# Performance work log

Hardware: AMD Instinct MI355X
Metric: run time of the kernel (lower is better)

Reference implementation:

```python
import jax, jax.numpy as jnp
import numpy as np

N_A = N_B = N_C = 50000
E = 800000
D_IN = 256
D_OUT = 128
T_ATT = 64


def _spmm(row, col, val, ft, n_dst):
    # sparse [n_dst, n_src] @ ft : gather src rows, scale, scatter-add to dst
    return jax.ops.segment_sum(val[:, None] * ft[col], row, num_segments=n_dst)


def setup_inputs() -> dict:
    key = jax.random.key(0)
    ks = jax.random.split(key, 40)
    f32 = jnp.float32
    inp = {
        'x_a': jax.random.normal(ks[0], (N_A, D_IN), f32),
        'x_b': jax.random.normal(ks[1], (N_B, D_IN), f32),
        'x_c': jax.random.normal(ks[2], (N_C, D_IN), f32),
    }
    # COO adjacency per relation: (dst_row, src_col, value)
    rel = {'ab': (N_A, N_B), 'ac': (N_A, N_C), 'ba': (N_B, N_A), 'ca': (N_C, N_A)}
    i = 3
    for name, (nd, ns) in rel.items():
        inp['row_' + name] = jax.random.randint(ks[i], (E,), 0, nd); i += 1
        inp['col_' + name] = jax.random.randint(ks[i], (E,), 0, ns); i += 1
        inp['val_' + name] = jax.random.uniform(ks[i], (E,), f32); i += 1
    # learned parameters (xavier-ish scale)
    def w(k, shape, s=0.05):
        return jax.random.normal(k, shape, f32) * s
    inp['w_self_a'] = w(ks[i], (D_IN, D_OUT)); i += 1
    inp['w_self_b'] = w(ks[i], (D_IN, D_OUT)); i += 1
    inp['w_self_c'] = w(ks[i], (D_IN, D_OUT)); i += 1
    inp['W_ab'] = w(ks[i], (D_IN, D_OUT)); i += 1
    inp['W_ac'] = w(ks[i], (D_IN, D_OUT)); i += 1
    inp['W_ba'] = w(ks[i], (D_IN, D_OUT)); i += 1
    inp['W_ca'] = w(ks[i], (D_IN, D_OUT)); i += 1
    inp['bias_a'] = w(ks[i], (1, D_OUT)); i += 1
    inp['bias_b'] = w(ks[i], (1, D_OUT)); i += 1
    inp['bias_c'] = w(ks[i], (1, D_OUT)); i += 1
    inp['w_cat_a'] = w(ks[i], (2 * D_OUT, D_OUT)); i += 1
    inp['w_cat_b'] = w(ks[i], (2 * D_OUT, D_OUT)); i += 1
    inp['w_cat_c'] = w(ks[i], (2 * D_OUT, D_OUT)); i += 1
    inp['w_query_a'] = w(ks[i], (D_OUT, T_ATT)); i += 1
    inp['w_keys_a'] = w(ks[i], (D_OUT, T_ATT)); i += 1
    inp['w_att_a'] = w(ks[i], (2 * T_ATT, 1)); i += 1
    return inp


def reference(x_a, x_b, x_c,
              row_ab, col_ab, val_ab, row_ac, col_ac, val_ac,
              row_ba, col_ba, val_ba, row_ca, col_ca, val_ca,
              w_self_a, w_self_b, w_self_c,
              W_ab, W_ac, W_ba, W_ca,
              bias_a, bias_b, bias_c,
              w_cat_a, w_cat_b, w_cat_c,
              w_query_a, w_keys_a, w_att_a):
    # ---- type 'a': neighbors [b, c], attention fusion ----
    self_a = x_a @ w_self_a                                   # [Na, D]
    nb_b = _spmm(row_ab, col_ab, val_ab, x_b @ W_ab, N_A)     # [Na, D]
    nb_c = _spmm(row_ac, col_ac, val_ac, x_c @ W_ac, N_A)     # [Na, D]
    q = self_a @ w_query_a                                    # [Na, T]
    e_b = jax.nn.elu(jnp.concatenate([nb_b @ w_keys_a, q], 1) @ w_att_a)  # [Na, 1]
    e_c = jax.nn.elu(jnp.concatenate([nb_c @ w_keys_a, q], 1) @ w_att_a)  # [Na, 1]
    att = jax.nn.softmax(jnp.concatenate([e_b, e_c], 1), axis=1)          # [Na, 2]
    agg_a = nb_b * att[:, :1] + nb_c * att[:, 1:2]
    out_a = jnp.concatenate([agg_a, self_a], 1) @ w_cat_a + bias_a
    # ---- type 'b': single neighbor 'a' ----
    self_b = x_b @ w_self_b
    agg_b = _spmm(row_ba, col_ba, val_ba, x_a @ W_ba, N_B)
    out_b = jnp.concatenate([agg_b, self_b], 1) @ w_cat_b + bias_b
    # ---- type 'c': single neighbor 'a' ----
    self_c = x_c @ w_self_c
    agg_c = _spmm(row_ca, col_ca, val_ca, x_a @ W_ca, N_C)
    out_c = jnp.concatenate([agg_c, self_c], 1) @ w_cat_c + bias_c
    # concat per-type outputs (all D_OUT wide) into one array
    return jnp.concatenate([out_a, out_b, out_c], 0)          # [Na+Nb+Nc, D]
```

## Files before the change

kernel.cpp:

```cpp
#include <hip/hip_runtime.h>

#define NA 50000
#define NE 800000
#define NBKT 196
#define CAP 4608
#define BSTRIDE (NBKT * CAP)

typedef unsigned int   u32;
typedef unsigned short u16;
typedef short s16x8 __attribute__((ext_vector_type(8)));
typedef float f32x4 __attribute__((ext_vector_type(4)));

__device__ __forceinline__ u16 f2bf(float f) {
  u32 u = __float_as_uint(f);
  u += 0x7fffu + ((u >> 16) & 1u);
  return (u16)(u >> 16);
}

__device__ __forceinline__ void acc8(float* a, uint4 q, float v) {
  a[0] += v * __uint_as_float(q.x << 16);
  a[1] += v * __uint_as_float(q.x & 0xffff0000u);
  a[2] += v * __uint_as_float(q.y << 16);
  a[3] += v * __uint_as_float(q.y & 0xffff0000u);
  a[4] += v * __uint_as_float(q.z << 16);
  a[5] += v * __uint_as_float(q.z & 0xffff0000u);
  a[6] += v * __uint_as_float(q.w << 16);
  a[7] += v * __uint_as_float(q.w & 0xffff0000u);
}

__device__ __forceinline__ void glds16(const u16* g, u16* l) {
  __builtin_amdgcn_global_load_lds(
      (const __attribute__((address_space(1))) u32*)g,
      (__attribute__((address_space(3))) u32*)l, 16, 0, 0);
}

struct Rel4 { const int* row[4]; const int* col[4]; const float* val[4]; };

struct Prep {
  const float* src[10]; u16* dst[10];
  const float* wq; const float* wk; const float* wa; float* uvp;
  u32* gcur;
};

struct ConvArgs { const float* x[3]; u16* xb; };

struct FtArgs { const u16* A[3]; const u16* Bt[3]; u16* C[3]; };

struct FuseW { const u16* Wf[3]; const float* bias[3]; float* out[3]; };

__global__ __launch_bounds__(256) void k_prep(Prep P) {
  int gy = blockIdx.y;
  if (gy < 7) {
    int idx = blockIdx.x * 256 + threadIdx.x;
    int k = idx & 255, n = idx >> 8;
    P.dst[gy][n * 256 + k] = f2bf(P.src[gy][k * 128 + n]);
  } else if (gy < 10) {
    int idx = blockIdx.x * 256 + threadIdx.x;
    int e = idx & 7, l = (idx >> 3) & 63, jj = (idx >> 9) & 7, ks = idx >> 12;
    int n = jj * 16 + (l & 15);
    int k = ks * 32 + ((l >> 4) * 8) + e;
    P.dst[gy][idx] = f2bf(P.src[gy][k * 128 + n]);
  } else if (blockIdx.x == 0) {
    int t = threadIdx.x;
    int d = t & 127, which = t >> 7;
    const float* w = which ? P.wq : P.wk;
    const float* a = P.wa + which * 64;
    float s = 0.f;
    for (int i = 0; i < 64; ++i) s += w[d * 64 + i] * a[i];
    P.uvp[which * 128 + d] = s;
  } else if (blockIdx.x == 1) {
    for (int i = threadIdx.x; i < 1024; i += 256)
      P.gcur[i] = (u32)((i & 255) * CAP);
  }
}

__global__ __launch_bounds__(256) void k_main1(Rel4 R, u32* __restrict__ gcur,
                                               uint2* __restrict__ pairs, ConvArgs CA) {
  __shared__ __align__(16) char smem[40960];
  const int gy = blockIdx.y;
  const int t = threadIdx.x;
  if (gy < 4) {
    if (blockIdx.x >= 196) return;
    int rel = gy;
    int e0 = blockIdx.x * 4096;
    int nrem = min(4096, NE - e0);
    u32* sw0  = (u32*)smem;
    u32* sval = sw0 + 4096;
    unsigned char* sbkt = (unsigned char*)(sval + 4096);
    u32* hist  = (u32*)(sbkt + 4096);
    u32* lscan = hist + 256;
    u32* cnt2  = lscan + 256;
    u32* gbase = cnt2 + 256;
    hist[t] = 0; cnt2[t] = 0;
    __syncthreads();
    const int* rr = R.row[rel];
    const int* cc = R.col[rel];
    const float* vl = R.val[rel];
    u32 w0[16]; u32 vv[16]; int bb[16];
    #pragma unroll
    for (int i = 0; i < 16; ++i) {
      int li = t + i * 256;
      bool ok = li < nrem;
      int idx = e0 + (ok ? li : 0);
      int r = ok ? rr[idx] : 0;
      int c = ok ? cc[idx] : 0;
      float v = ok ? vl[idx] : 0.f;
      u32 b = (u32)r >> 8;
      w0[i] = (u32)(c & 0xFFFF) | ((u32)(r & 255) << 16) | (b << 24);
      vv[i] = __float_as_uint(v);
      bb[i] = ok ? (int)b : -1;
      if (ok) atomicAdd(&hist[b], 1u);
    }
    __syncthreads();
    lscan[t] = hist[t];
    __syncthreads();
    for (int ofs = 1; ofs < 256; ofs <<= 1) {
      u32 y = (t >= ofs) ? lscan[t - ofs] : 0u;
      __syncthreads();
      lscan[t] += y;
      __syncthreads();
    }
    gbase[t] = atomicAdd(&gcur[rel * 256 + t], hist[t]);
    #pragma unroll
    for (int i = 0; i < 16; ++i) {
      if (bb[i] >= 0) {
        int b = bb[i];
        u32 p = (lscan[b] - hist[b]) + atomicAdd(&cnt2[b], 1u);
        sw0[p] = w0[i]; sval[p] = vv[i]; sbkt[p] = (unsigned char)b;
      }
    }
    __syncthreads();
    uint2* P = pairs + (size_t)rel * BSTRIDE;
    #pragma unroll
    for (int i = 0; i < 16; ++i) {
      int p = t + i * 256;
      if (p < nrem) {
        int b = sbkt[p];
        u32 gd = gbase[b] + (u32)p - (lscan[b] - hist[b]);
        uint2 pr; pr.x = sw0[p]; pr.y = sval[p];
        P[gd] = pr;
      }
    }
  } else {
    const size_t TOT = 38400000;
    const size_t TSZ = 12800000;
    size_t base = ((size_t)(gy - 4) * 391 + blockIdx.x) * 16384 + (size_t)t * 8;
    #pragma unroll
    for (int it = 0; it < 8; ++it) {
      size_t g = base + (size_t)it * 2048;
      if (g < TOT) {
        int which = (g >= 2 * TSZ) ? 2 : (g >= TSZ ? 1 : 0);
        size_t off = g - (size_t)which * TSZ;
        const float* sp = CA.x[which] + off;
        float4 v0 = *(const float4*)(sp);
        float4 v1 = *(const float4*)(sp + 4);
        s16x8 o;
        o[0] = (short)f2bf(v0.x); o[1] = (short)f2bf(v0.y);
        o[2] = (short)f2bf(v0.z); o[3] = (short)f2bf(v0.w);
        o[4] = (short)f2bf(v1.x); o[5] = (short)f2bf(v1.y);
        o[6] = (short)f2bf(v1.z); o[7] = (short)f2bf(v1.w);
        *(s16x8*)(CA.xb + g) = o;
      }
    }
  }
}

__global__ __launch_bounds__(256) void k_main2(const u32* __restrict__ gcur,
    int* __restrict__ ofs_s, int* __restrict__ ofs_e,
    const uint2* __restrict__ pairs, u32* __restrict__ epak, FtArgs Ar) {
  __shared__ __align__(16) char smem[40960];
  const int gy = blockIdx.y;
  const int t = threadIdx.x;
  if (gy < 4) {
    if (blockIdx.x >= 196) return;
    int rel = gy;
    int b = blockIdx.x;
    int base = b * CAP;
    int n = (int)gcur[rel * 256 + b] - base;
    u32* sw0  = (u32*)smem;
    u32* sv   = sw0 + CAP;
    u32* hist = sv + CAP;
    u32* scan = hist + 256;
    u32* cur  = scan + 256;
    hist[t] = 0;
    __syncthreads();
    const uint2* P = pairs + (size_t)rel * BSTRIDE;
    for (int p = t; p < n; p += 256) {
      uint2 pr = P[base + p];
      sw0[p] = pr.x; sv[p] = pr.y;
      atomicAdd(&hist[(pr.x >> 16) & 255], 1u);
    }
    __syncthreads();
    u32 own = hist[t];
    scan[t] = own;
    __syncthreads();
    for (int ofs = 1; ofs < 256; ofs <<= 1) {
      u32 y = (t >= ofs) ? scan[t - ofs] : 0u;
      __syncthreads();
      scan[t] += y;
      __syncthreads();
    }
    u32 excl = scan[t] - own;
    cur[t] = excl;
    int r0 = b << 8;
    if (r0 + t < NA) {
      ofs_s[(size_t)rel * NA + r0 + t] = base + (int)excl;
      ofs_e[(size_t)rel * NA + r0 + t] = base + (int)(excl + own);
    }
    __syncthreads();
    u32* E = epak + (size_t)rel * BSTRIDE;
    for (int p = t; p < n; p += 256) {
      u32 w = sw0[p];
      int rl = (w >> 16) & 255;
      u32 d = atomicAdd(&cur[rl], 1u);
      E[base + (int)d] = (w & 0xFFFFu) | ((u32)f2bf(__uint_as_float(sv[p])) << 16);
    }
  } else {
    u16* Asl = (u16*)smem;
    u16* Bsl = Asl + 128 * 64;
    const int by = gy - 4;
    const int which = (by < 3) ? 0 : (by < 5 ? 1 : 2);
    const int col0 = (by - (which == 0 ? 0 : (which == 1 ? 3 : 5))) * 128;
    const int ldc = (which == 0) ? 384 : 256;
    const u16* A = Ar.A[which];
    const u16* Bt = Ar.Bt[which] + (size_t)col0 * 256;
    u16* C = Ar.C[which] + col0;
    const int row0 = blockIdx.x * 128;
    const int w = t >> 6, l = t & 63;
    const int wr = (w >> 1) * 64, wc = (w & 1) * 64;
    f32x4 acc[4][4] = {};
    for (int kk = 0; kk < 4; ++kk) {
      #pragma unroll
      for (int q = 0; q < 4; ++q) {
        int c = q * 256 + t;
        int r = c >> 3, col8 = (c & 7) * 8;
        int gr = row0 + r; gr = gr < NA ? gr : NA - 1;
        glds16(A + (size_t)gr * 256 + kk * 64 + col8, Asl + c * 8);
        glds16(Bt + (size_t)r * 256 + kk * 64 + col8, Bsl + c * 8);
      }
      __syncthreads();
      #pragma unroll
      for (int ks = 0; ks < 2; ++ks) {
        s16x8 af[4], bfr[4];
        #pragma unroll
        for (int i = 0; i < 4; ++i)
          af[i] = *(const s16x8*)&Asl[(wr + i * 16 + (l & 15)) * 64 + ks * 32 + (l >> 4) * 8];
        #pragma unroll
        for (int j = 0; j < 4; ++j)
          bfr[j] = *(const s16x8*)&Bsl[(wc + j * 16 + (l & 15)) * 64 + ks * 32 + (l >> 4) * 8];
        #pragma unroll
        for (int i = 0; i < 4; ++i)
          #pragma unroll
          for (int j = 0; j < 4; ++j)
            acc[i][j] = __builtin_amdgcn_mfma_f32_16x16x32_bf16(af[i], bfr[j], acc[i][j], 0, 0, 0);
      }
      __syncthreads();
    }
    #pragma unroll
    for (int i = 0; i < 4; ++i)
      #pragma unroll
      for (int j = 0; j < 4; ++j)
        #pragma unroll
        for (int q = 0; q < 4; ++q) {
          int r = row0 + wr + i * 16 + (l >> 4) * 4 + q;
          if (r < NA) C[(size_t)r * ldc + wc + j * 16 + (l & 15)] = f2bf(acc[i][j][q]);
        }
  }
}

__global__ __launch_bounds__(256) void k_spmm(
    const int* __restrict__ ofs_s, const int* __restrict__ ofs_e,
    const u32* __restrict__ epak,
    const u16* __restrict__ ya, const u16* __restrict__ yb, const u16* __restrict__ yc,
    const float* __restrict__ uv, FuseW FW) {
  __shared__ u16 Asm[16 * 264];
  int tid = threadIdx.x;
  int lane = tid & 63, wid = tid >> 6;
  int g = lane >> 4, gl = lane & 15;
  const u32 glb = (u32)gl * 16;
  int lr = wid * 4 + g;
  int row = blockIdx.x * 16 + lr;
  int gy = blockIdx.y;
  if (gy == 0) {
    const char* ybase = (const char*)yb;
    const char* cbase = (const char*)yc;
    float fb[8] = {0,0,0,0,0,0,0,0};
    float fc[8] = {0,0,0,0,0,0,0,0};
    {
      int i = ofs_s[row], e = ofs_e[row];
      for (; i + 4 <= e; i += 4) {
        u32 p0 = epak[i], p1 = epak[i + 1], p2 = epak[i + 2], p3 = epak[i + 3];
        uint4 q0 = *(const uint4*)(ybase + (((p0 & 0xFFFFu) << 9) + glb));
        uint4 q1 = *(const uint4*)(ybase + (((p1 & 0xFFFFu) << 9) + glb));
        uint4 q2 = *(const uint4*)(ybase + (((p2 & 0xFFFFu) << 9) + glb));
        uint4 q3 = *(const uint4*)(ybase + (((p3 & 0xFFFFu) << 9) + glb));
        acc8(fb, q0, __uint_as_float(p0 & 0xffff0000u));
        acc8(fb, q1, __uint_as_float(p1 & 0xffff0000u));
        acc8(fb, q2, __uint_as_float(p2 & 0xffff0000u));
        acc8(fb, q3, __uint_as_float(p3 & 0xffff0000u));
      }
      for (; i < e; ++i) {
        u32 p0 = epak[i];
        uint4 q0 = *(const uint4*)(ybase + (((p0 & 0xFFFFu) << 9) + glb));
        acc8(fb, q0, __uint_as_float(p0 & 0xffff0000u));
      }
    }
    {
      const u32* pr = epak + BSTRIDE;
      int i = ofs_s[NA + row], e = ofs_e[NA + row];
      for (; i + 4 <= e; i += 4) {
        u32 p0 = pr[i], p1 = pr[i + 1], p2 = pr[i + 2], p3 = pr[i + 3];
        uint4 q0 = *(const uint4*)(cbase + (((p0 & 0xFFFFu) << 9) + glb));
        uint4 q1 = *(const uint4*)(cbase + (((p1 & 0xFFFFu) << 9) + glb));
        uint4 q2 = *(const uint4*)(cbase + (((p2 & 0xFFFFu) << 9) + glb));
        uint4 q3 = *(const uint4*)(cbase + (((p3 & 0xFFFFu) << 9) + glb));
        acc8(fc, q0, __uint_as_float(p0 & 0xffff0000u));
        acc8(fc, q1, __uint_as_float(p1 & 0xffff0000u));
        acc8(fc, q2, __uint_as_float(p2 & 0xffff0000u));
        acc8(fc, q3, __uint_as_float(p3 & 0xffff0000u));
      }
      for (; i < e; ++i) {
        u32 p0 = pr[i];
        uint4 q0 = *(const uint4*)(cbase + (((p0 & 0xFFFFu) << 9) + glb));
        acc8(fc, q0, __uint_as_float(p0 & 0xffff0000u));
      }
    }
    uint4 sq = *(const uint4*)((const char*)ya + (u32)row * 768 + glb);
    float sf[8];
    sf[0] = __uint_as_float(sq.x << 16); sf[1] = __uint_as_float(sq.x & 0xffff0000u);
    sf[2] = __uint_as_float(sq.y << 16); sf[3] = __uint_as_float(sq.y & 0xffff0000u);
    sf[4] = __uint_as_float(sq.z << 16); sf[5] = __uint_as_float(sq.z & 0xffff0000u);
    sf[6] = __uint_as_float(sq.w << 16); sf[7] = __uint_as_float(sq.w & 0xffff0000u);
    float pb = 0.f, pc = 0.f, pq = 0.f;
    const float* up = uv + gl * 8;
    const float* vp = uv + 128 + gl * 8;
    #pragma unroll
    for (int j = 0; j < 8; ++j) {
      pb += fb[j] * up[j];
      pc += fc[j] * up[j];
      pq += sf[j] * vp[j];
    }
    #pragma unroll
    for (int off = 1; off < 16; off <<= 1) {
      pb += __shfl_xor(pb, off);
      pc += __shfl_xor(pc, off);
      pq += __shfl_xor(pq, off);
    }
    float eb = pb + pq, ec = pc + pq;
    eb = eb > 0.f ? eb : (expf(eb) - 1.f);
    ec = ec > 0.f ? ec : (expf(ec) - 1.f);
    float m = fmaxf(eb, ec);
    float p0 = expf(eb - m), p1 = expf(ec - m);
    float inv = 1.f / (p0 + p1);
    float a0 = p0 * inv, a1 = p1 * inv;
    s16x8 av;
    #pragma unroll
    for (int j = 0; j < 8; ++j) av[j] = (short)f2bf(a0 * fb[j] + a1 * fc[j]);
    *(s16x8*)&Asm[lr * 264 + gl * 8] = av;
    *(s16x8*)&Asm[lr * 264 + 128 + gl * 8] = *(s16x8*)&sq;
  } else {
    const int which = gy - 1;
    const int* os = ofs_s + (2 + which) * NA;
    const int* oe = ofs_e + (2 + which) * NA;
    const u32* pr = epak + (size_t)(2 + which) * BSTRIDE;
    const char* fbase = (const char*)ya + (which ? 512 : 256);
    const char* selfp = (const char*)(which ? yc : yb);
    float fa[8] = {0,0,0,0,0,0,0,0};
    int i = os[row], e = oe[row];
    for (; i + 4 <= e; i += 4) {
      u32 p0 = pr[i], p1 = pr[i + 1], p2 = pr[i + 2], p3 = pr[i + 3];
      uint4 q0 = *(const uint4*)(fbase + ((p0 & 0xFFFFu) * 768u + glb));
      uint4 q1 = *(const uint4*)(fbase + ((p1 & 0xFFFFu) * 768u + glb));
      uint4 q2 = *(const uint4*)(fbase + ((p2 & 0xFFFFu) * 768u + glb));
      uint4 q3 = *(const uint4*)(fbase + ((p3 & 0xFFFFu) * 768u + glb));
      acc8(fa, q0, __uint_as_float(p0 & 0xffff0000u));
      acc8(fa, q1, __uint_as_float(p1 & 0xffff0000u));
      acc8(fa, q2, __uint_as_float(p2 & 0xffff0000u));
      acc8(fa, q3, __uint_as_float(p3 & 0xffff0000u));
    }
    for (; i < e; ++i) {
      u32 p0 = pr[i];
      uint4 q0 = *(const uint4*)(fbase + ((p0 & 0xFFFFu) * 768u + glb));
      acc8(fa, q0, __uint_as_float(p0 & 0xffff0000u));
    }
    s16x8 av;
    #pragma unroll
    for (int j = 0; j < 8; ++j) av[j] = (short)f2bf(fa[j]);
    *(s16x8*)&Asm[lr * 264 + gl * 8] = av;
    *(s16x8*)&Asm[lr * 264 + 128 + gl * 8] =
        *(const s16x8*)(selfp + (u32)row * 512 + 256 + glb);
  }
  __syncthreads();
  const u16* Wf = FW.Wf[gy];
  const float* bias = FW.bias[gy];
  float* outp = FW.out[gy];
  const int j0 = wid * 2, j1 = wid * 2 + 1;
  f32x4 acc0 = {0.f, 0.f, 0.f, 0.f}, acc1 = {0.f, 0.f, 0.f, 0.f};
  #pragma unroll
  for (int ks = 0; ks < 8; ++ks) {
    s16x8 a = *(const s16x8*)&Asm[(lane & 15) * 264 + ks * 32 + (lane >> 4) * 8];
    s16x8 b0 = *(const s16x8*)(Wf + ((size_t)(ks * 8 + j0) * 64 + lane) * 8);
    s16x8 b1 = *(const s16x8*)(Wf + ((size_t)(ks * 8 + j1) * 64 + lane) * 8);
    acc0 = __builtin_amdgcn_mfma_f32_16x16x32_bf16(a, b0, acc0, 0, 0, 0);
    acc1 = __builtin_amdgcn_mfma_f32_16x16x32_bf16(a, b1, acc1, 0, 0, 0);
  }
  const int c0 = j0 * 16 + (lane & 15), c1 = j1 * 16 + (lane & 15);
  const float b0v = bias[c0], b1v = bias[c1];
  const int rbase = blockIdx.x * 16 + (lane >> 4) * 4;
  #pragma unroll
  for (int q = 0; q < 4; ++q) {
    outp[(size_t)(rbase + q) * 128 + c0] = acc0[q] + b0v;
    outp[(size_t)(rbase + q) * 128 + c1] = acc1[q] + b1v;
  }
}

extern "C" void kernel_launch(void* const* d_in, const int* in_sizes, int n_in,
                              void* d_out, int out_size, void* d_ws, size_t ws_size,
                              hipStream_t stream) {
  const float* x_a = (const float*)d_in[0];
  const float* x_b = (const float*)d_in[1];
  const float* x_c = (const float*)d_in[2];
  const int* row_ab = (const int*)d_in[3];
  const int* col_ab = (const int*)d_in[4];
  const float* val_ab = (const float*)d_in[5];
  const int* row_ac = (const int*)d_in[6];
  const int* col_ac = (const int*)d_in[7];
  const float* val_ac = (const float*)d_in[8];
  const int* row_ba = (const int*)d_in[9];
  const int* col_ba = (const int*)d_in[10];
  const float* val_ba = (const float*)d_in[11];
  const int* row_ca = (const int*)d_in[12];
  const int* col_ca = (const int*)d_in[13];
  const float* val_ca = (const float*)d_in[14];
  const float* w_self_a = (const float*)d_in[15];
  const float* w_self_b = (const float*)d_in[16];
  const float* w_self_c = (const float*)d_in[17];
  const float* W_ab = (const float*)d_in[18];
  const float* W_ac = (const float*)d_in[19];
  const float* W_ba = (const float*)d_in[20];
  const float* W_ca = (const float*)d_in[21];
  const float* bias_a = (const float*)d_in[22];
  const float* bias_b = (const float*)d_in[23];
  const float* bias_c = (const float*)d_in[24];
  const float* w_cat_a = (const float*)d_in[25];
  const float* w_cat_b = (const float*)d_in[26];
  const float* w_cat_c = (const float*)d_in[27];
  const float* w_query_a = (const float*)d_in[28];
  const float* w_keys_a = (const float*)d_in[29];
  const float* w_att_a = (const float*)d_in[30];

  float* out = (float*)d_out;

  char* ws = (char*)d_ws;
  size_t off_b = 0;
  auto walloc = [&](size_t bytes) {
    void* p = ws + off_b;
    off_b = (off_b + bytes + 255) & ~(size_t)255;
    return p;
  };
  u16* ya = (u16*)walloc((size_t)NA * 384 * 2);
  u16* yb = (u16*)walloc((size_t)NA * 256 * 2);
  u16* yc = (u16*)walloc((size_t)NA * 256 * 2);
  int* ofs_s = (int*)walloc((size_t)4 * NA * 4);
  int* ofs_e = (int*)walloc((size_t)4 * NA * 4);
  u32* gcur = (u32*)walloc((size_t)4 * 256 * 4);
  uint2* pairs = (uint2*)walloc((size_t)4 * BSTRIDE * 8);
  u32* epak = (u32*)walloc((size_t)4 * BSTRIDE * 4);
  u16* Wa_t = (u16*)walloc((size_t)384 * 256 * 2);
  u16* Wb_t = (u16*)walloc((size_t)256 * 256 * 2);
  u16* Wc_t = (u16*)walloc((size_t)256 * 256 * 2);
  u16* Wcat_a = (u16*)walloc((size_t)128 * 256 * 2);
  u16* Wcat_b = (u16*)walloc((size_t)128 * 256 * 2);
  u16* Wcat_c = (u16*)walloc((size_t)128 * 256 * 2);
  float* uvbuf = (float*)walloc(256 * 4);
  u16* xb = (u16*)walloc((size_t)3 * NA * 256 * 2);

  Rel4 R;
  R.row[0] = row_ab; R.col[0] = col_ab; R.val[0] = val_ab;
  R.row[1] = row_ac; R.col[1] = col_ac; R.val[1] = val_ac;
  R.row[2] = row_ba; R.col[2] = col_ba; R.val[2] = val_ba;
  R.row[3] = row_ca; R.col[3] = col_ca; R.val[3] = val_ca;

  Prep P;
  P.src[0] = w_self_a; P.dst[0] = Wa_t;
  P.src[1] = W_ba;     P.dst[1] = Wa_t + 128 * 256;
  P.src[2] = W_ca;     P.dst[2] = Wa_t + 256 * 256;
  P.src[3] = W_ab;     P.dst[3] = Wb_t;
  P.src[4] = w_self_b; P.dst[4] = Wb_t + 128 * 256;
  P.src[5] = W_ac;     P.dst[5] = Wc_t;
  P.src[6] = w_self_c; P.dst[6] = Wc_t + 128 * 256;
  P.src[7] = w_cat_a;  P.dst[7] = Wcat_a;
  P.src[8] = w_cat_b;  P.dst[8] = Wcat_b;
  P.src[9] = w_cat_c;  P.dst[9] = Wcat_c;
  P.wq = w_query_a; P.wk = w_keys_a; P.wa = w_att_a; P.uvp = uvbuf;
  P.gcur = gcur;

  dim3 gp(128, 11);
  k_prep<<<gp, 256, 0, stream>>>(P);

  ConvArgs CA;
  CA.x[0] = x_a; CA.x[1] = x_b; CA.x[2] = x_c;
  CA.xb = xb;
  dim3 g1(391, 11);
  k_main1<<<g1, 256, 0, stream>>>(R, gcur, pairs, CA);

  FtArgs FA;
  FA.A[0] = xb; FA.A[1] = xb + (size_t)NA * 256; FA.A[2] = xb + (size_t)2 * NA * 256;
  FA.Bt[0] = Wa_t; FA.Bt[1] = Wb_t; FA.Bt[2] = Wc_t;
  FA.C[0] = ya; FA.C[1] = yb; FA.C[2] = yc;
  dim3 g2(391, 11);
  k_main2<<<g2, 256, 0, stream>>>(gcur, ofs_s, ofs_e, pairs, epak, FA);

  FuseW FW;
  FW.Wf[0] = Wcat_a; FW.Wf[1] = Wcat_b; FW.Wf[2] = Wcat_c;
  FW.bias[0] = bias_a; FW.bias[1] = bias_b; FW.bias[2] = bias_c;
  FW.out[0] = out; FW.out[1] = out + (size_t)NA * 128; FW.out[2] = out + (size_t)NA * 128 * 2;
  dim3 gs(3125, 3);
  k_spmm<<<gs, 256, 0, stream>>>(ofs_s, ofs_e, epak, ya, yb, yc, uvbuf, FW);
}
```

Measured before the change: 269.4 us.

## Fold weight prep into main1 and use packed f32x2 accumulation in spmm

Removes the separate k_prep launch. Weight transposes, bf16 conversion and the attention-vector precompute now run as an extra grid row of k_main1, and the bucket cursors are zeroed with hipMemsetAsync and offset by bucket base at use sites. The gather-accumulate loops in k_spmm switch to f32x2 vector arithmetic so the compiler can emit packed FMA instructions. This saves one kernel launch and its serialization, at the cost of a memset call and reliance on weights being ready before k_main2 consumes them.

```diff
diff --git a/kernel.cpp b/kernel.cpp
--- a/kernel.cpp
+++ b/kernel.cpp
@@ -10,6 +10,7 @@
 typedef unsigned short u16;
 typedef short s16x8 __attribute__((ext_vector_type(8)));
 typedef float f32x4 __attribute__((ext_vector_type(4)));
+typedef float f32x2 __attribute__((ext_vector_type(2)));
 
 __device__ __forceinline__ u16 f2bf(float f) {
   u32 u = __float_as_uint(f);
@@ -17,15 +18,17 @@
   return (u16)(u >> 16);
 }
 
-__device__ __forceinline__ void acc8(float* a, uint4 q, float v) {
-  a[0] += v * __uint_as_float(q.x << 16);
-  a[1] += v * __uint_as_float(q.x & 0xffff0000u);
-  a[2] += v * __uint_as_float(q.y << 16);
-  a[3] += v * __uint_as_float(q.y & 0xffff0000u);
-  a[4] += v * __uint_as_float(q.z << 16);
-  a[5] += v * __uint_as_float(q.z & 0xffff0000u);
-  a[6] += v * __uint_as_float(q.w << 16);
-  a[7] += v * __uint_as_float(q.w & 0xffff0000u);
+__device__ __forceinline__ void accp8(f32x2* a, uint4 q, float v) {
+  f32x2 vv; vv[0] = v; vv[1] = v;
+  f32x2 f;
+  f[0] = __uint_as_float(q.x << 16); f[1] = __uint_as_float(q.x & 0xffff0000u);
+  a[0] += vv * f;
+  f[0] = __uint_as_float(q.y << 16); f[1] = __uint_as_float(q.y & 0xffff0000u);
+  a[1] += vv * f;
+  f[0] = __uint_as_float(q.z << 16); f[1] = __uint_as_float(q.z & 0xffff0000u);
+  a[2] += vv * f;
+  f[0] = __uint_as_float(q.w << 16); f[1] = __uint_as_float(q.w & 0xffff0000u);
+  a[3] += vv * f;
 }
 
 __device__ __forceinline__ void glds16(const u16* g, u16* l) {
@@ -39,7 +42,6 @@
 struct Prep {
   const float* src[10]; u16* dst[10];
   const float* wq; const float* wk; const float* wa; float* uvp;
-  u32* gcur;
 };
 
 struct ConvArgs { const float* x[3]; u16* xb; };
@@ -48,34 +50,9 @@
 
 struct FuseW { const u16* Wf[3]; const float* bias[3]; float* out[3]; };
 
-__global__ __launch_bounds__(256) void k_prep(Prep P) {
-  int gy = blockIdx.y;
-  if (gy < 7) {
-    int idx = blockIdx.x * 256 + threadIdx.x;
-    int k = idx & 255, n = idx >> 8;
-    P.dst[gy][n * 256 + k] = f2bf(P.src[gy][k * 128 + n]);
-  } else if (gy < 10) {
-    int idx = blockIdx.x * 256 + threadIdx.x;
-    int e = idx & 7, l = (idx >> 3) & 63, jj = (idx >> 9) & 7, ks = idx >> 12;
-    int n = jj * 16 + (l & 15);
-    int k = ks * 32 + ((l >> 4) * 8) + e;
-    P.dst[gy][idx] = f2bf(P.src[gy][k * 128 + n]);
-  } else if (blockIdx.x == 0) {
-    int t = threadIdx.x;
-    int d = t & 127, which = t >> 7;
-    const float* w = which ? P.wq : P.wk;
-    const float* a = P.wa + which * 64;
-    float s = 0.f;
-    for (int i = 0; i < 64; ++i) s += w[d * 64 + i] * a[i];
-    P.uvp[which * 128 + d] = s;
-  } else if (blockIdx.x == 1) {
-    for (int i = threadIdx.x; i < 1024; i += 256)
-      P.gcur[i] = (u32)((i & 255) * CAP);
-  }
-}
-
 __global__ __launch_bounds__(256) void k_main1(Rel4 R, u32* __restrict__ gcur,
-                                               uint2* __restrict__ pairs, ConvArgs CA) {
+                                               uint2* __restrict__ pairs, ConvArgs CA,
+                                               Prep P) {
   __shared__ __align__(16) char smem[40960];
   const int gy = blockIdx.y;
   const int t = threadIdx.x;
@@ -120,7 +97,7 @@
       lscan[t] += y;
       __syncthreads();
     }
-    gbase[t] = atomicAdd(&gcur[rel * 256 + t], hist[t]);
+    gbase[t] = (u32)t * CAP + atomicAdd(&gcur[rel * 256 + t], hist[t]);
     #pragma unroll
     for (int i = 0; i < 16; ++i) {
       if (bb[i] >= 0) {
@@ -130,7 +107,7 @@
       }
     }
     __syncthreads();
-    uint2* P = pairs + (size_t)rel * BSTRIDE;
+    uint2* Pp = pairs + (size_t)rel * BSTRIDE;
     #pragma unroll
     for (int i = 0; i < 16; ++i) {
       int p = t + i * 256;
@@ -138,10 +115,10 @@
         int b = sbkt[p];
         u32 gd = gbase[b] + (u32)p - (lscan[b] - hist[b]);
         uint2 pr; pr.x = sw0[p]; pr.y = sval[p];
-        P[gd] = pr;
-      }
-    }
-  } else {
+        Pp[gd] = pr;
+      }
+    }
+  } else if (gy < 11) {
     const size_t TOT = 38400000;
     const size_t TSZ = 12800000;
     size_t base = ((size_t)(gy - 4) * 391 + blockIdx.x) * 16384 + (size_t)t * 8;
@@ -162,6 +139,32 @@
         *(s16x8*)(CA.xb + g) = o;
       }
     }
+  } else {
+    const int bx = blockIdx.x;
+    if (bx < 320) {
+      #pragma unroll
+      for (int rep = 0; rep < 4; ++rep) {
+        int idx = bx * 1024 + rep * 256 + t;
+        int w = idx >> 15;
+        int r = idx & 32767;
+        if (w < 7) {
+          int k = r & 255, n = r >> 8;
+          P.dst[w][n * 256 + k] = f2bf(P.src[w][k * 128 + n]);
+        } else {
+          int e = r & 7, l = (r >> 3) & 63, jj = (r >> 9) & 7, ks = r >> 12;
+          int n = jj * 16 + (l & 15);
+          int k = ks * 32 + ((l >> 4) * 8) + e;
+          P.dst[w][r] = f2bf(P.src[w][k * 128 + n]);
+        }
+      }
+    } else if (bx == 320) {
+      int d = t & 127, which = t >> 7;
+      const float* w = which ? P.wq : P.wk;
+      const float* a = P.wa + which * 64;
+      float s = 0.f;
+      for (int i = 0; i < 64; ++i) s += w[d * 64 + i] * a[i];
+      P.uvp[which * 128 + d] = s;
+    }
   }
 }
 
@@ -176,7 +179,7 @@
     int rel = gy;
     int b = blockIdx.x;
     int base = b * CAP;
-    int n = (int)gcur[rel * 256 + b] - base;
+    int n = (int)gcur[rel * 256 + b];
     u32* sw0  = (u32*)smem;
     u32* sv   = sw0 + CAP;
     u32* hist = sv + CAP;
@@ -284,8 +287,7 @@
   if (gy == 0) {
     const char* ybase = (const char*)yb;
     const char* cbase = (const char*)yc;
-    float fb[8] = {0,0,0,0,0,0,0,0};
-    float fc[8] = {0,0,0,0,0,0,0,0};
+    f32x2 fb2[4] = {}; f32x2 fc2[4] = {};
     {
       int i = ofs_s[row], e = ofs_e[row];
       for (; i + 4 <= e; i += 4) {
@@ -294,15 +296,15 @@
         uint4 q1 = *(const uint4*)(ybase + (((p1 & 0xFFFFu) << 9) + glb));
         uint4 q2 = *(const uint4*)(ybase + (((p2 & 0xFFFFu) << 9) + glb));
         uint4 q3 = *(const uint4*)(ybase + (((p3 & 0xFFFFu) << 9) + glb));
-        acc8(fb, q0, __uint_as_float(p0 & 0xffff0000u));
-        acc8(fb, q1, __uint_as_float(p1 & 0xffff0000u));
-        acc8(fb, q2, __uint_as_float(p2 & 0xffff0000u));
-        acc8(fb, q3, __uint_as_float(p3 & 0xffff0000u));
+        accp8(fb2, q0, __uint_as_float(p0 & 0xffff0000u));
+        accp8(fb2, q1, __uint_as_float(p1 & 0xffff0000u));
+        accp8(fb2, q2, __uint_as_float(p2 & 0xffff0000u));
+        accp8(fb2, q3, __uint_as_float(p3 & 0xffff0000u));
       }
       for (; i < e; ++i) {
         u32 p0 = epak[i];
         uint4 q0 = *(const uint4*)(ybase + (((p0 & 0xFFFFu) << 9) + glb));
-        acc8(fb, q0, __uint_as_float(p0 & 0xffff0000u));
+        accp8(fb2, q0, __uint_as_float(p0 & 0xffff0000u));
       }
     }
     {
@@ -314,17 +316,20 @@
         uint4 q1 = *(const uint4*)(cbase + (((p1 & 0xFFFFu) << 9) + glb));
         uint4 q2 = *(const uint4*)(cbase + (((p2 & 0xFFFFu) << 9) + glb));
         uint4 q3 = *(const uint4*)(cbase + (((p3 & 0xFFFFu) << 9) + glb));
-        acc8(fc, q0, __uint_as_float(p0 & 0xffff0000u));
-        acc8(fc, q1, __uint_as_float(p1 & 0xffff0000u));
-        acc8(fc, q2, __uint_as_float(p2 & 0xffff0000u));
-        acc8(fc, q3, __uint_as_float(p3 & 0xffff0000u));
+        accp8(fc2, q0, __uint_as_float(p0 & 0xffff0000u));
+        accp8(fc2, q1, __uint_as_float(p1 & 0xffff0000u));
+        accp8(fc2, q2, __uint_as_float(p2 & 0xffff0000u));
+        accp8(fc2, q3, __uint_as_float(p3 & 0xffff0000u));
       }
       for (; i < e; ++i) {
         u32 p0 = pr[i];
         uint4 q0 = *(const uint4*)(cbase + (((p0 & 0xFFFFu) << 9) + glb));
-        acc8(fc, q0, __uint_as_float(p0 & 0xffff0000u));
-      }
-    }
+        accp8(fc2, q0, __uint_as_float(p0 & 0xffff0000u));
+      }
+    }
+    float fb[8], fc[8];
+    #pragma unroll
+    for (int j = 0; j < 8; ++j) { fb[j] = fb2[j >> 1][j & 1]; fc[j] = fc2[j >> 1][j & 1]; }
     uint4 sq = *(const uint4*)((const char*)ya + (u32)row * 768 + glb);
     float sf[8];
     sf[0] = __uint_as_float(sq.x << 16); sf[1] = __uint_as_float(sq.x & 0xffff0000u);
@@ -365,7 +370,7 @@
     const u32* pr = epak + (size_t)(2 + which) * BSTRIDE;
     const char* fbase = (const char*)ya + (which ? 512 : 256);
     const char* selfp = (const char*)(which ? yc : yb);
-    float fa[8] = {0,0,0,0,0,0,0,0};
+    f32x2 fa2[4] = {};
     int i = os[row], e = oe[row];
     for (; i + 4 <= e; i += 4) {
       u32 p0 = pr[i], p1 = pr[i + 1], p2 = pr[i + 2], p3 = pr[i + 3];
@@ -373,19 +378,19 @@
       uint4 q1 = *(const uint4*)(fbase + ((p1 & 0xFFFFu) * 768u + glb));
       uint4 q2 = *(const uint4*)(fbase + ((p2 & 0xFFFFu) * 768u + glb));
       uint4 q3 = *(const uint4*)(fbase + ((p3 & 0xFFFFu) * 768u + glb));
-      acc8(fa, q0, __uint_as_float(p0 & 0xffff0000u));
-      acc8(fa, q1, __uint_as_float(p1 & 0xffff0000u));
-      acc8(fa, q2, __uint_as_float(p2 & 0xffff0000u));
-      acc8(fa, q3, __uint_as_float(p3 & 0xffff0000u));
+      accp8(fa2, q0, __uint_as_float(p0 & 0xffff0000u));
+      accp8(fa2, q1, __uint_as_float(p1 & 0xffff0000u));
+      accp8(fa2, q2, __uint_as_float(p2 & 0xffff0000u));
+      accp8(fa2, q3, __uint_as_float(p3 & 0xffff0000u));
     }
     for (; i < e; ++i) {
       u32 p0 = pr[i];
       uint4 q0 = *(const uint4*)(fbase + ((p0 & 0xFFFFu) * 768u + glb));
-      acc8(fa, q0, __uint_as_float(p0 & 0xffff0000u));
+      accp8(fa2, q0, __uint_as_float(p0 & 0xffff0000u));
     }
     s16x8 av;
     #pragma unroll
-    for (int j = 0; j < 8; ++j) av[j] = (short)f2bf(fa[j]);
+    for (int j = 0; j < 8; ++j) av[j] = (short)f2bf(fa2[j >> 1][j & 1]);
     *(s16x8*)&Asm[lr * 264 + gl * 8] = av;
     *(s16x8*)&Asm[lr * 264 + 128 + gl * 8] =
         *(const s16x8*)(selfp + (u32)row * 512 + 256 + glb);
@@ -493,16 +498,14 @@
   P.src[8] = w_cat_b;  P.dst[8] = Wcat_b;
   P.src[9] = w_cat_c;  P.dst[9] = Wcat_c;
   P.wq = w_query_a; P.wk = w_keys_a; P.wa = w_att_a; P.uvp = uvbuf;
-  P.gcur = gcur;
-
-  dim3 gp(128, 11);
-  k_prep<<<gp, 256, 0, stream>>>(P);
+
+  hipMemsetAsync(gcur, 0, (size_t)4 * 256 * 4, stream);
 
   ConvArgs CA;
   CA.x[0] = x_a; CA.x[1] = x_b; CA.x[2] = x_c;
   CA.xb = xb;
-  dim3 g1(391, 11);
-  k_main1<<<g1, 256, 0, stream>>>(R, gcur, pairs, CA);
+  dim3 g1(391, 12);
+  k_main1<<<g1, 256, 0, stream>>>(R, gcur, pairs, CA, P);
 
   FtArgs FA;
   FA.A[0] = xb; FA.A[1] = xb + (size_t)NA * 256; FA.A[2] = xb + (size_t)2 * NA * 256;
```

After: 266.1 us. About the same (-1.2%).
